# Optimization experiments

Measured on AMD Instinct MI355X. Metric: run time of the kernel, lower is better.

## Reference

```python
import jax, jax.numpy as jnp
import numpy as np

N_NODES = 100000
N_EDGES = 1600000
IN_CH = 128
HID = 128
OUT_CH = 10
NUM_LAYERS = 3
NUM_GRAPHS = 512


def _glorot(key, shape):
    fan_in, fan_out = shape[0], shape[1]
    lim = jnp.sqrt(6.0 / (fan_in + fan_out))
    return jax.random.uniform(key, shape, jnp.float32, -lim, lim)


def setup_inputs() -> dict:
    key = jax.random.key(0)
    ks = jax.random.split(key, 20)
    inp = {}
    inp["x"] = jax.random.normal(ks[0], (N_NODES, IN_CH), jnp.float32)
    inp["edge_index"] = jax.random.randint(ks[1], (2, N_EDGES), 0, N_NODES, jnp.int64)
    inp["batch"] = jnp.sort(jax.random.randint(ks[2], (N_NODES,), 0, NUM_GRAPHS, jnp.int64))
    # GIN layer MLP params: Linear(in, hid) -> ReLU -> Linear(hid, hid)
    kidx = 3
    for l in range(NUM_LAYERS):
        d_in = IN_CH if l == 0 else HID
        inp[f"w1_{l}"] = _glorot(ks[kidx], (d_in, HID)); kidx += 1
        inp[f"b1_{l}"] = jnp.zeros((HID,), jnp.float32)
        inp[f"w2_{l}"] = _glorot(ks[kidx], (HID, HID)); kidx += 1
        inp[f"b2_{l}"] = jnp.zeros((HID,), jnp.float32)
    inp["lin_w"] = _glorot(ks[kidx], (HID, OUT_CH))
    inp["lin_b"] = jnp.zeros((OUT_CH,), jnp.float32)
    return inp


def _gin_forward(x, src, dst, batch, layer_params, lin_w, lin_b):
    h = x
    n_layers = len(layer_params)
    for i, (w1, b1, w2, b2) in enumerate(layer_params):
        # GINConv: (1 + eps) * h + sum_{j in N(i)} h_j, eps = 0
        agg = jax.ops.segment_sum(h[src], dst, num_segments=N_NODES)
        z = h + agg
        # MLP: Linear -> ReLU -> Linear
        h = jnp.maximum(z @ w1 + b1, 0.0) @ w2 + b2
        if i < n_layers - 1:  # inter-layer ReLU (PyG BasicGNN act)
            h = jnp.maximum(h, 0.0)
    # global_add_pool over batch ids -> [NUM_GRAPHS, HID]
    pooled = jax.ops.segment_sum(h, batch, num_segments=NUM_GRAPHS)
    # dropout(p=0.5) is identity in eval mode
    return pooled @ lin_w + lin_b


def reference(x, edge_index, batch,
              w1_0, b1_0, w2_0, b2_0,
              w1_1, b1_1, w2_1, b2_1,
              w1_2, b1_2, w2_2, b2_2,
              lin_w, lin_b):
    src, dst = edge_index[0], edge_index[1]
    layer_params = [(w1_0, b1_0, w2_0, b2_0),
                    (w1_1, b1_1, w2_1, b2_1),
                    (w1_2, b1_2, w2_2, b2_2)]
    return _gin_forward(x, src, dst, batch, layer_params, lin_w, lin_b)
```

## Files before the change

kernel.cpp:

```cpp
#include <hip/hip_runtime.h>

#define CH 128
#define OUTC 10
#define NB2 512
#define BSHIFT 8
#define BCAP2 5120
#define PCHUNK 2048
#define PQ2 132
#define FBM 64

typedef __attribute__((ext_vector_type(8))) short short8;
typedef __attribute__((ext_vector_type(4))) short short4v;
typedef __attribute__((ext_vector_type(16))) float f32x16;
typedef __attribute__((ext_vector_type(2))) float f32x2;


__device__ inline unsigned short f2bf(float f) {
    unsigned u = __builtin_bit_cast(unsigned, f);
    u += 0x7fffu + ((u >> 16) & 1u);
    return (unsigned short)(u >> 16);
}
__device__ inline float bflo(unsigned u) { return __builtin_bit_cast(float, u << 16); }
__device__ inline float bfhi(unsigned u) { return __builtin_bit_cast(float, u & 0xffff0000u); }

__device__ inline f32x2 bf2(unsigned u) {
    return (f32x2){__builtin_bit_cast(float, u << 16),
                   __builtin_bit_cast(float, u & 0xffff0000u)};
}

__device__ inline void acc8(f32x2* a, const uint4& v) {
    a[0] += bf2(v.x);
    a[1] += bf2(v.y);
    a[2] += bf2(v.z);
    a[3] += bf2(v.w);
}


struct WPtrs { const float* s[6]; unsigned short* d[6]; };

__global__ void prep_part_kernel(const int* __restrict__ src, const int* __restrict__ dst,
                                 int* __restrict__ bucketCnt, unsigned* __restrict__ pairs, int E,
                                 int nPartBlk,
                                 const float4* __restrict__ x4, uint2* __restrict__ xb, int n4,
                                 int nConvBlk, WPtrs p,
                                 uint4* __restrict__ pooled4, int nPooled4) {
    __shared__ int hist[NB2];
    __shared__ int base[NB2];
    __shared__ int cur[NB2];
    int tid = threadIdx.x;
    int b = blockIdx.x;

    if (b < nPartBlk) {
        int e0 = b * PCHUNK;
        hist[tid] = 0; hist[tid + 256] = 0;
        __syncthreads();
        #pragma unroll
        for (int i = 0; i < PCHUNK / 256; ++i) {
            int e = e0 + tid + i * 256;
            if (e < E) atomicAdd(&hist[dst[e] >> BSHIFT], 1);
        }
        __syncthreads();
        #pragma unroll
        for (int k = 0; k < 2; ++k) {
            int t2 = tid + k * 256;
            int c = hist[t2];
            base[t2] = (c > 0) ? atomicAdd(&bucketCnt[t2], c) : 0;
            cur[t2] = 0;
        }
        __syncthreads();
        #pragma unroll
        for (int i = 0; i < PCHUNK / 256; ++i) {
            int e = e0 + tid + i * 256;
            if (e < E) {
                int d = dst[e];
                int bkt = d >> BSHIFT;
                int pos = base[bkt] + atomicAdd(&cur[bkt], 1);
                if (pos < BCAP2)
                    pairs[bkt * BCAP2 + pos] = ((unsigned)(d & 255) << 17) | (unsigned)src[e];
            }
        }
    } else if (b < nPartBlk + nConvBlk) {
        int i = (b - nPartBlk) * 256 + tid;
        if (i < n4) {
            float4 v = x4[i];
            uint2 o;
            o.x = (unsigned)f2bf(v.x) | ((unsigned)f2bf(v.y) << 16);
            o.y = (unsigned)f2bf(v.z) | ((unsigned)f2bf(v.w) << 16);
            xb[i] = o;
        }
    } else if (b < nPartBlk + nConvBlk + 384) {
        int bb = b - nPartBlk - nConvBlk;
        int m = bb >> 6;
        int i = (bb & 63) * 256 + tid;
        int j = i & 7;
        int l = (i >> 3) & 63;
        int k0 = (i >> 9) & 7;
        int ct = (i >> 12) & 3;
        int k = k0 * 16 + ((l >> 5) << 3) + j;
        int nn = ct * 32 + (l & 31);
        p.d[m][i] = f2bf(p.s[m][k * CH + nn]);
    } else {
        int i = (b - nPartBlk - nConvBlk - 384) * 256 + tid;
        if (i < nPooled4) pooled4[i] = make_uint4(0, 0, 0, 0);
    }
}


__launch_bounds__(512)
__global__ void build_csr_kernel(const unsigned* __restrict__ pairs, const int* __restrict__ bucketCnt,
                                 int* __restrict__ offs, int* __restrict__ csr, int N) {
    __shared__ int bsm[NB2];
    __shared__ int ldeg[256];
    __shared__ int s0[256], s1[256];
    __shared__ int lexc[256];
    __shared__ int lcur[256];
    __shared__ int lcsr[BCAP2];

    int b = blockIdx.x;
    int node0 = b << BSHIFT;
    if (node0 >= N) return;
    int nLocal = min(256, N - node0);
    int tid = threadIdx.x;

    bsm[tid] = bucketCnt[tid];
    __syncthreads();
    for (int off = 1; off < NB2; off <<= 1) {
        int t = (tid >= off) ? bsm[tid - off] : 0;
        __syncthreads();
        bsm[tid] += t;
        __syncthreads();
    }
    int cnt = min(bucketCnt[b], BCAP2);
    int gbase = bsm[b] - bucketCnt[b];

    if (tid < 256) ldeg[tid] = 0;
    __syncthreads();
    for (int i = tid; i < cnt; i += 512)
        atomicAdd(&ldeg[pairs[b * BCAP2 + i] >> 17], 1);
    __syncthreads();

    if (tid < 256) s0[tid] = ldeg[tid];
    __syncthreads();
    int* sp = s0; int* dp = s1;
    for (int off = 1; off < 256; off <<= 1) {
        if (tid < 256) dp[tid] = sp[tid] + ((tid >= off) ? sp[tid - off] : 0);
        __syncthreads();
        int* t = sp; sp = dp; dp = t;
    }
    if (tid < 256) {
        int ex = sp[tid] - ldeg[tid];
        lexc[tid] = ex;
        lcur[tid] = ex;
    }
    __syncthreads();

    for (int i = tid; i < cnt; i += 512) {
        unsigned w = pairs[b * BCAP2 + i];
        int ppos = atomicAdd(&lcur[w >> 17], 1);
        lcsr[ppos] = (int)(w & 0x1ffffu);
    }
    __syncthreads();

    for (int i = tid; i < cnt; i += 512) csr[gbase + i] = lcsr[i];
    for (int i = tid; i < nLocal; i += 512) offs[node0 + i] = gbase + lexc[i];
    if (tid == 0 && node0 + nLocal == N) offs[N] = gbase + cnt;
}


template <int L, int RELU, int POOL>
__launch_bounds__(512)
__global__ void fused_gin_kernel(const uint4* __restrict__ h4,
                                 const int* __restrict__ offs, const int* __restrict__ csr,
                                 const unsigned short* __restrict__ w1s, const float* __restrict__ b1,
                                 const unsigned short* __restrict__ w2s, const float* __restrict__ b2,
                                 unsigned short* __restrict__ hout,
                                 const int* __restrict__ batch, float* __restrict__ pooled,
                                 int n) {
    __shared__ __align__(16) unsigned short zs[FBM * PQ2];

    int tid = threadIdx.x;
    int row0 = blockIdx.x * FBM;

    {
        int gl = tid & 15;
        int grp = tid >> 4;
        #pragma unroll
        for (int it = 0; it < 2; ++it) {
            int rr = grp + 32 * it;
            int node = row0 + rr;
            unsigned o0 = 0, o1 = 0, o2 = 0, o3 = 0;
            if (node < n) {
                int beg = offs[node], end = offs[node + 1];
                f32x2 a[4];
                uint4 self = h4[node * 16 + gl];
                a[0] = bf2(self.x);
                a[1] = bf2(self.y);
                a[2] = bf2(self.z);
                a[3] = bf2(self.w);
                int e = beg;
                int elim = beg + ((end - beg) & ~3);
                if (e < elim) {
                    int s0 = csr[e], s1 = csr[e + 1], s2 = csr[e + 2], s3 = csr[e + 3];
                    for (; e + 8 <= elim; e += 4) {
                        uint4 v0 = h4[s0 * 16 + gl];
                        uint4 v1 = h4[s1 * 16 + gl];
                        uint4 v2 = h4[s2 * 16 + gl];
                        uint4 v3 = h4[s3 * 16 + gl];
                        int t0 = csr[e + 4], t1 = csr[e + 5], t2 = csr[e + 6], t3 = csr[e + 7];
                        acc8(a, v0); acc8(a, v1); acc8(a, v2); acc8(a, v3);
                        s0 = t0; s1 = t1; s2 = t2; s3 = t3;
                    }
                    {
                        uint4 v0 = h4[s0 * 16 + gl];
                        uint4 v1 = h4[s1 * 16 + gl];
                        uint4 v2 = h4[s2 * 16 + gl];
                        uint4 v3 = h4[s3 * 16 + gl];
                        acc8(a, v0); acc8(a, v1); acc8(a, v2); acc8(a, v3);
                        e += 4;
                    }
                }
                for (; e < end; ++e) {
                    uint4 v = h4[csr[e] * 16 + gl];
                    acc8(a, v);
                }
                o0 = (unsigned)f2bf(a[0][0]) | ((unsigned)f2bf(a[0][1]) << 16);
                o1 = (unsigned)f2bf(a[1][0]) | ((unsigned)f2bf(a[1][1]) << 16);
                o2 = (unsigned)f2bf(a[2][0]) | ((unsigned)f2bf(a[2][1]) << 16);
                o3 = (unsigned)f2bf(a[3][0]) | ((unsigned)f2bf(a[3][1]) << 16);
            }
            *(uint2*)&zs[rr * PQ2 + gl * 8]     = make_uint2(o0, o1);
            *(uint2*)&zs[rr * PQ2 + gl * 8 + 4] = make_uint2(o2, o3);
        }
    }
    __syncthreads();

    int wv = tid >> 6;
    int lane = tid & 63;
    int l31 = lane & 31;
    int kh = lane >> 5;
    int rt = wv & 1;
    int ct = wv >> 1;
    int arow = rt * 32 + l31;

    f32x16 acc;
    {
        float bv = b1[ct * 32 + l31];
        #pragma unroll
        for (int r = 0; r < 16; ++r) acc[r] = bv;
    }
    #pragma unroll
    for (int k0 = 0; k0 < 8; ++k0) {
        short8 afr;
        {
            short4v lo = *(const short4v*)&zs[arow * PQ2 + k0 * 16 + kh * 8];
            short4v hi = *(const short4v*)&zs[arow * PQ2 + k0 * 16 + kh * 8 + 4];
            afr = (short8){lo[0], lo[1], lo[2], lo[3], hi[0], hi[1], hi[2], hi[3]};
        }
        short8 bfr = *(const short8*)&w1s[(((ct * 8 + k0) * 64) + lane) * 8];
        acc = __builtin_amdgcn_mfma_f32_32x32x16_bf16(afr, bfr, acc, 0, 0, 0);
    }
    __syncthreads();

    #pragma unroll
    for (int reg = 0; reg < 16; ++reg) {
        int crow = (reg & 3) + 8 * (reg >> 2) + 4 * kh;
        zs[(rt * 32 + crow) * PQ2 + ct * 32 + l31] = f2bf(fmaxf(acc[reg], 0.f));
    }
    __syncthreads();

    {
        float bv = b2[ct * 32 + l31];
        #pragma unroll
        for (int r = 0; r < 16; ++r) acc[r] = bv;
    }
    #pragma unroll
    for (int k0 = 0; k0 < 8; ++k0) {
        short8 afr;
        {
            short4v lo = *(const short4v*)&zs[arow * PQ2 + k0 * 16 + kh * 8];
            short4v hi = *(const short4v*)&zs[arow * PQ2 + k0 * 16 + kh * 8 + 4];
            afr = (short8){lo[0], lo[1], lo[2], lo[3], hi[0], hi[1], hi[2], hi[3]};
        }
        short8 bfr = *(const short8*)&w2s[(((ct * 8 + k0) * 64) + lane) * 8];
        acc = __builtin_amdgcn_mfma_f32_32x32x16_bf16(afr, bfr, acc, 0, 0, 0);
    }
    __syncthreads();

    #pragma unroll
    for (int reg = 0; reg < 16; ++reg) {
        int crow = (reg & 3) + 8 * (reg >> 2) + 4 * kh;
        float v = acc[reg];
        if (RELU) v = fmaxf(v, 0.f);
        zs[(rt * 32 + crow) * PQ2 + ct * 32 + l31] = f2bf(v);
    }
    __syncthreads();

    if (!POOL) {
        for (int i = tid; i < FBM * 16; i += 512) {
            int r = i >> 4, c = i & 15;
            int row = row0 + r;
            if (row < n) {
                uint2 a2 = *(const uint2*)&zs[r * PQ2 + c * 8];
                uint2 b2v = *(const uint2*)&zs[r * PQ2 + c * 8 + 4];
                ((uint4*)hout)[row * 16 + c] = make_uint4(a2.x, a2.y, b2v.x, b2v.y);
            }
        }
    } else {
        int c2 = tid & 63;
        int rs = tid >> 6;
        float a0 = 0.f, a1 = 0.f;
        int prevg = -1;
        #pragma unroll
        for (int i = 0; i < FBM / 8; ++i) {
            int r = rs + 8 * i;
            int row = row0 + r;
            if (row >= n) break;
            int g = batch[row];
            if (g != prevg) {
                if (prevg >= 0) {
                    atomicAdd(&pooled[prevg * CH + 2 * c2], a0);
                    atomicAdd(&pooled[prevg * CH + 2 * c2 + 1], a1);
                }
                prevg = g; a0 = 0.f; a1 = 0.f;
            }
            unsigned v = *(const unsigned*)&zs[r * PQ2 + c2 * 2];
            a0 += bflo(v); a1 += bfhi(v);
        }
        if (prevg >= 0) {
            atomicAdd(&pooled[prevg * CH + 2 * c2], a0);
            atomicAdd(&pooled[prevg * CH + 2 * c2 + 1], a1);
        }
    }
}


__global__ void final_linear_kernel(const float* __restrict__ pooled, const float* __restrict__ lin_w,
                                    const float* __restrict__ lin_b, float* __restrict__ out) {
    int g = blockIdx.x;
    int tid = threadIdx.x;
    __shared__ float pl[CH];
    pl[tid] = pooled[g * CH + tid];
    __syncthreads();
    if (tid < OUTC) {
        float a = lin_b[tid];
        #pragma unroll 16
        for (int c = 0; c < CH; ++c) a = fmaf(pl[c], lin_w[c * OUTC + tid], a);
        out[g * OUTC + tid] = a;
    }
}


static inline size_t aln(size_t x) { return (x + 255) & ~size_t(255); }

extern "C" void kernel_launch(void* const* d_in, const int* in_sizes, int n_in,
                              void* d_out, int out_size, void* d_ws, size_t ws_size,
                              hipStream_t stream) {
    const float* x      = (const float*)d_in[0];
    const int*   ei     = (const int*)d_in[1];
    const int*   batch  = (const int*)d_in[2];
    const float* w1[3]  = {(const float*)d_in[3], (const float*)d_in[7],  (const float*)d_in[11]};
    const float* b1[3]  = {(const float*)d_in[4], (const float*)d_in[8],  (const float*)d_in[12]};
    const float* w2[3]  = {(const float*)d_in[5], (const float*)d_in[9],  (const float*)d_in[13]};
    const float* b2[3]  = {(const float*)d_in[6], (const float*)d_in[10], (const float*)d_in[14]};
    const float* lin_w  = (const float*)d_in[15];
    const float* lin_b  = (const float*)d_in[16];
    float* out = (float*)d_out;

    int E = in_sizes[1] / 2;
    int N = in_sizes[2];
    int n_graphs = out_size / OUTC;
    const int* src = ei;
    const int* dst = ei + E;

    char* p = (char*)d_ws;
    int* bucketCnt  = (int*)p; p += aln(NB2 * 4);
    unsigned* pairs = (unsigned*)p; p += aln((size_t)NB2 * BCAP2 * 4);
    int* offs       = (int*)p; p += aln((size_t)(N + 1) * 4);
    int* csr        = (int*)p; p += aln((size_t)E * 4);
    unsigned short* xb = (unsigned short*)p; p += aln((size_t)N * CH * 2);
    unsigned short* hA = (unsigned short*)p; p += aln((size_t)N * CH * 2);
    unsigned short* hB = (unsigned short*)p; p += aln((size_t)N * CH * 2);
    float* pooled = (float*)p; p += aln((size_t)n_graphs * CH * 4);
    unsigned short* wt[6];
    for (int i = 0; i < 6; ++i) { wt[i] = (unsigned short*)p; p += aln((size_t)CH * CH * 2); }
    (void)ws_size; (void)n_in;

    hipMemsetAsync(bucketCnt, 0, NB2 * 4, stream);

    int n4 = N * CH / 4;
    int nConvBlk = (n4 + 255) / 256;
    int nPartBlk = (E + PCHUNK - 1) / PCHUNK;
    int nPooled4 = n_graphs * CH / 4;
    int nZeroBlk = (nPooled4 + 255) / 256;
    WPtrs wp;
    for (int l = 0; l < 3; ++l) {
        wp.s[2 * l] = w1[l];     wp.d[2 * l] = wt[2 * l];
        wp.s[2 * l + 1] = w2[l]; wp.d[2 * l + 1] = wt[2 * l + 1];
    }
    prep_part_kernel<<<nPartBlk + nConvBlk + 384 + nZeroBlk, 256, 0, stream>>>(
        src, dst, bucketCnt, pairs, E, nPartBlk,
        (const float4*)x, (uint2*)xb, n4, nConvBlk, wp,
        (uint4*)pooled, nPooled4);

    build_csr_kernel<<<NB2, 512, 0, stream>>>(pairs, bucketCnt, offs, csr, N);

    int fblk = (N + FBM - 1) / FBM;

    fused_gin_kernel<0, 1, 0><<<fblk, 512, 0, stream>>>((const uint4*)xb, offs, csr,
        wt[0], b1[0], wt[1], b2[0], hA, batch, pooled, N);
    fused_gin_kernel<1, 1, 0><<<fblk, 512, 0, stream>>>((const uint4*)hA, offs, csr,
        wt[2], b1[1], wt[3], b2[1], hB, batch, pooled, N);
    fused_gin_kernel<2, 0, 1><<<fblk, 512, 0, stream>>>((const uint4*)hB, offs, csr,
        wt[4], b1[2], wt[5], b2[2], (unsigned short*)nullptr, batch, pooled, N);

    final_linear_kernel<<<n_graphs, CH, 0, stream>>>(pooled, lin_w, lin_b, out);
}
```

Measured before the change: 377.1 us.

## Merge all GIN stages into one persistent cooperative kernel with grid syncs

Replaces the six separate launches (partition/prep, CSR build, three fused GIN layers, final linear) with a single cooperative persistent kernel. Grid-wide syncs separate the stages, and blocks loop over work items in grid-stride fashion. The aim is to remove per-launch overhead and the tail gaps between kernels. The cost is lower occupancy: shared memory is sized for the largest stage, and the grid is capped by the occupancy query. It also adds grid-sync overhead, and the aggregation loop drops its software-pipelined csr prefetch.

Measured after the change: 872.9 us. +131.5%, slower.

```diff
diff --git a/kernel.cpp b/kernel.cpp
--- a/kernel.cpp
+++ b/kernel.cpp
@@ -1,4 +1,7 @@
 #include <hip/hip_runtime.h>
+#include <hip/hip_cooperative_groups.h>
+
+namespace cg = cooperative_groups;
 
 #define CH 128
 #define OUTC 10
@@ -8,6 +11,7 @@
 #define PCHUNK 2048
 #define PQ2 132
 #define FBM 64
+#define TPB 512
 
 typedef __attribute__((ext_vector_type(8))) short short8;
 typedef __attribute__((ext_vector_type(4))) short short4v;
@@ -36,203 +40,158 @@
 }
 
 
-struct WPtrs { const float* s[6]; unsigned short* d[6]; };
-
-__global__ void prep_part_kernel(const int* __restrict__ src, const int* __restrict__ dst,
-                                 int* __restrict__ bucketCnt, unsigned* __restrict__ pairs, int E,
-                                 int nPartBlk,
-                                 const float4* __restrict__ x4, uint2* __restrict__ xb, int n4,
-                                 int nConvBlk, WPtrs p,
-                                 uint4* __restrict__ pooled4, int nPooled4) {
-    __shared__ int hist[NB2];
-    __shared__ int base[NB2];
-    __shared__ int cur[NB2];
+struct MegaP {
+    const int* src; const int* dst; int E;
+    int* bucketCnt; unsigned* pairs;
+    int* offs; int* csr; int N;
+    const float4* x4; unsigned short* xb; int n4;
+    const float* wsrc[6]; unsigned short* wdst[6];
+    const float* b1v[3]; const float* b2v[3];
+    unsigned short* hA; unsigned short* hB;
+    const int* batch; float* pooled; int nPooled4;
+    int nGraphs; const float* lin_w; const float* lin_b; float* out;
+};
+
+
+__launch_bounds__(TPB, 8)
+__global__ void mega_kernel(MegaP P) {
+    cg::grid_group gg = cg::this_grid();
+    __shared__ __align__(16) int smem[6912];
+
     int tid = threadIdx.x;
     int b = blockIdx.x;
-
-    if (b < nPartBlk) {
-        int e0 = b * PCHUNK;
-        hist[tid] = 0; hist[tid + 256] = 0;
+    int grid = (int)gridDim.x;
+
+    int nPartBlk = (P.E + PCHUNK - 1) / PCHUNK;
+    for (int pb = b; pb < nPartBlk; pb += grid) {
+        int* hist = smem;
+        int* base = smem + NB2;
+        int* cur  = smem + 2 * NB2;
+        int e0 = pb * PCHUNK;
+        hist[tid] = 0;
         __syncthreads();
         #pragma unroll
-        for (int i = 0; i < PCHUNK / 256; ++i) {
-            int e = e0 + tid + i * 256;
-            if (e < E) atomicAdd(&hist[dst[e] >> BSHIFT], 1);
+        for (int i = 0; i < PCHUNK / TPB; ++i) {
+            int e = e0 + tid + i * TPB;
+            if (e < P.E) atomicAdd(&hist[P.dst[e] >> BSHIFT], 1);
+        }
+        __syncthreads();
+        {
+            int c = hist[tid];
+            base[tid] = (c > 0) ? atomicAdd(&P.bucketCnt[tid], c) : 0;
+            cur[tid] = 0;
         }
         __syncthreads();
         #pragma unroll
-        for (int k = 0; k < 2; ++k) {
-            int t2 = tid + k * 256;
-            int c = hist[t2];
-            base[t2] = (c > 0) ? atomicAdd(&bucketCnt[t2], c) : 0;
-            cur[t2] = 0;
-        }
-        __syncthreads();
-        #pragma unroll
-        for (int i = 0; i < PCHUNK / 256; ++i) {
-            int e = e0 + tid + i * 256;
-            if (e < E) {
-                int d = dst[e];
+        for (int i = 0; i < PCHUNK / TPB; ++i) {
+            int e = e0 + tid + i * TPB;
+            if (e < P.E) {
+                int d = P.dst[e];
                 int bkt = d >> BSHIFT;
                 int pos = base[bkt] + atomicAdd(&cur[bkt], 1);
                 if (pos < BCAP2)
-                    pairs[bkt * BCAP2 + pos] = ((unsigned)(d & 255) << 17) | (unsigned)src[e];
-            }
-        }
-    } else if (b < nPartBlk + nConvBlk) {
-        int i = (b - nPartBlk) * 256 + tid;
-        if (i < n4) {
-            float4 v = x4[i];
+                    P.pairs[bkt * BCAP2 + pos] = ((unsigned)(d & 255) << 17) | (unsigned)P.src[e];
+            }
+        }
+        __syncthreads();
+    }
+    {
+        int wtot = 6 * 16384 + P.nPooled4;
+        int rb = grid - 1 - b;
+        for (int i = rb * TPB + tid; i < wtot; i += grid * TPB) {
+            if (i < 6 * 16384) {
+                int m = i >> 14;
+                int im = i & 16383;
+                int j = im & 7;
+                int l = (im >> 3) & 63;
+                int k0 = (im >> 9) & 7;
+                int ct = (im >> 12) & 3;
+                int k = k0 * 16 + ((l >> 5) << 3) + j;
+                int nn = ct * 32 + (l & 31);
+                P.wdst[m][im] = f2bf(P.wsrc[m][k * CH + nn]);
+            } else {
+                ((uint4*)P.pooled)[i - 6 * 16384] = make_uint4(0, 0, 0, 0);
+            }
+        }
+    }
+    gg.sync();
+
+    int nCsr = (P.N + 255) >> BSHIFT;
+    for (int cb = b; cb < nCsr; cb += grid) {
+        int* bsm  = smem;
+        int* ldeg = smem + NB2;
+        int* s0   = smem + NB2 + 256;
+        int* s1   = s0 + 256;
+        int* lexc = s1 + 256;
+        int* lcur = lexc + 256;
+        int* lcsr = lcur + 256;
+        int node0 = cb << BSHIFT;
+        int nLocal = min(256, P.N - node0);
+
+        bsm[tid] = P.bucketCnt[tid];
+        __syncthreads();
+        for (int off = 1; off < NB2; off <<= 1) {
+            int t = (tid >= off) ? bsm[tid - off] : 0;
+            __syncthreads();
+            bsm[tid] += t;
+            __syncthreads();
+        }
+        int cnt = min(P.bucketCnt[cb], BCAP2);
+        int gbase = bsm[cb] - P.bucketCnt[cb];
+
+        if (tid < 256) ldeg[tid] = 0;
+        __syncthreads();
+        for (int i = tid; i < cnt; i += TPB)
+            atomicAdd(&ldeg[P.pairs[cb * BCAP2 + i] >> 17], 1);
+        __syncthreads();
+
+        if (tid < 256) s0[tid] = ldeg[tid];
+        __syncthreads();
+        int* sp = s0; int* dp = s1;
+        for (int off = 1; off < 256; off <<= 1) {
+            if (tid < 256) dp[tid] = sp[tid] + ((tid >= off) ? sp[tid - off] : 0);
+            __syncthreads();
+            int* t = sp; sp = dp; dp = t;
+        }
+        if (tid < 256) {
+            int ex = sp[tid] - ldeg[tid];
+            lexc[tid] = ex;
+            lcur[tid] = ex;
+        }
+        __syncthreads();
+
+        for (int i = tid; i < cnt; i += TPB) {
+            unsigned w = P.pairs[cb * BCAP2 + i];
+            int ppos = atomicAdd(&lcur[w >> 17], 1);
+            lcsr[ppos] = (int)(w & 0x1ffffu);
+        }
+        __syncthreads();
+
+        for (int i = tid; i < cnt; i += TPB) P.csr[gbase + i] = lcsr[i];
+        for (int i = tid; i < nLocal; i += TPB) P.offs[node0 + i] = gbase + lexc[i];
+        if (tid == 0 && node0 + nLocal == P.N) P.offs[P.N] = gbase + cnt;
+        __syncthreads();
+    }
+    {
+        int i0, stride;
+        if (grid > nCsr) {
+            if (b >= nCsr) { i0 = (b - nCsr) * TPB + tid; stride = (grid - nCsr) * TPB; }
+            else           { i0 = P.n4; stride = 1; }
+        } else {
+            i0 = b * TPB + tid; stride = grid * TPB;
+        }
+        for (int i = i0; i < P.n4; i += stride) {
+            float4 v = P.x4[i];
             uint2 o;
             o.x = (unsigned)f2bf(v.x) | ((unsigned)f2bf(v.y) << 16);
             o.y = (unsigned)f2bf(v.z) | ((unsigned)f2bf(v.w) << 16);
-            xb[i] = o;
-        }
-    } else if (b < nPartBlk + nConvBlk + 384) {
-        int bb = b - nPartBlk - nConvBlk;
-        int m = bb >> 6;
-        int i = (bb & 63) * 256 + tid;
-        int j = i & 7;
-        int l = (i >> 3) & 63;
-        int k0 = (i >> 9) & 7;
-        int ct = (i >> 12) & 3;
-        int k = k0 * 16 + ((l >> 5) << 3) + j;
-        int nn = ct * 32 + (l & 31);
-        p.d[m][i] = f2bf(p.s[m][k * CH + nn]);
-    } else {
-        int i = (b - nPartBlk - nConvBlk - 384) * 256 + tid;
-        if (i < nPooled4) pooled4[i] = make_uint4(0, 0, 0, 0);
-    }
-}
-
-
-__launch_bounds__(512)
-__global__ void build_csr_kernel(const unsigned* __restrict__ pairs, const int* __restrict__ bucketCnt,
-                                 int* __restrict__ offs, int* __restrict__ csr, int N) {
-    __shared__ int bsm[NB2];
-    __shared__ int ldeg[256];
-    __shared__ int s0[256], s1[256];
-    __shared__ int lexc[256];
-    __shared__ int lcur[256];
-    __shared__ int lcsr[BCAP2];
-
-    int b = blockIdx.x;
-    int node0 = b << BSHIFT;
-    if (node0 >= N) return;
-    int nLocal = min(256, N - node0);
-    int tid = threadIdx.x;
-
-    bsm[tid] = bucketCnt[tid];
-    __syncthreads();
-    for (int off = 1; off < NB2; off <<= 1) {
-        int t = (tid >= off) ? bsm[tid - off] : 0;
-        __syncthreads();
-        bsm[tid] += t;
-        __syncthreads();
-    }
-    int cnt = min(bucketCnt[b], BCAP2);
-    int gbase = bsm[b] - bucketCnt[b];
-
-    if (tid < 256) ldeg[tid] = 0;
-    __syncthreads();
-    for (int i = tid; i < cnt; i += 512)
-        atomicAdd(&ldeg[pairs[b * BCAP2 + i] >> 17], 1);
-    __syncthreads();
-
-    if (tid < 256) s0[tid] = ldeg[tid];
-    __syncthreads();
-    int* sp = s0; int* dp = s1;
-    for (int off = 1; off < 256; off <<= 1) {
-        if (tid < 256) dp[tid] = sp[tid] + ((tid >= off) ? sp[tid - off] : 0);
-        __syncthreads();
-        int* t = sp; sp = dp; dp = t;
-    }
-    if (tid < 256) {
-        int ex = sp[tid] - ldeg[tid];
-        lexc[tid] = ex;
-        lcur[tid] = ex;
-    }
-    __syncthreads();
-
-    for (int i = tid; i < cnt; i += 512) {
-        unsigned w = pairs[b * BCAP2 + i];
-        int ppos = atomicAdd(&lcur[w >> 17], 1);
-        lcsr[ppos] = (int)(w & 0x1ffffu);
-    }
-    __syncthreads();
-
-    for (int i = tid; i < cnt; i += 512) csr[gbase + i] = lcsr[i];
-    for (int i = tid; i < nLocal; i += 512) offs[node0 + i] = gbase + lexc[i];
-    if (tid == 0 && node0 + nLocal == N) offs[N] = gbase + cnt;
-}
-
-
-template <int L, int RELU, int POOL>
-__launch_bounds__(512)
-__global__ void fused_gin_kernel(const uint4* __restrict__ h4,
-                                 const int* __restrict__ offs, const int* __restrict__ csr,
-                                 const unsigned short* __restrict__ w1s, const float* __restrict__ b1,
-                                 const unsigned short* __restrict__ w2s, const float* __restrict__ b2,
-                                 unsigned short* __restrict__ hout,
-                                 const int* __restrict__ batch, float* __restrict__ pooled,
-                                 int n) {
-    __shared__ __align__(16) unsigned short zs[FBM * PQ2];
-
-    int tid = threadIdx.x;
-    int row0 = blockIdx.x * FBM;
-
-    {
-        int gl = tid & 15;
-        int grp = tid >> 4;
-        #pragma unroll
-        for (int it = 0; it < 2; ++it) {
-            int rr = grp + 32 * it;
-            int node = row0 + rr;
-            unsigned o0 = 0, o1 = 0, o2 = 0, o3 = 0;
-            if (node < n) {
-                int beg = offs[node], end = offs[node + 1];
-                f32x2 a[4];
-                uint4 self = h4[node * 16 + gl];
-                a[0] = bf2(self.x);
-                a[1] = bf2(self.y);
-                a[2] = bf2(self.z);
-                a[3] = bf2(self.w);
-                int e = beg;
-                int elim = beg + ((end - beg) & ~3);
-                if (e < elim) {
-                    int s0 = csr[e], s1 = csr[e + 1], s2 = csr[e + 2], s3 = csr[e + 3];
-                    for (; e + 8 <= elim; e += 4) {
-                        uint4 v0 = h4[s0 * 16 + gl];
-                        uint4 v1 = h4[s1 * 16 + gl];
-                        uint4 v2 = h4[s2 * 16 + gl];
-                        uint4 v3 = h4[s3 * 16 + gl];
-                        int t0 = csr[e + 4], t1 = csr[e + 5], t2 = csr[e + 6], t3 = csr[e + 7];
-                        acc8(a, v0); acc8(a, v1); acc8(a, v2); acc8(a, v3);
-                        s0 = t0; s1 = t1; s2 = t2; s3 = t3;
-                    }
-                    {
-                        uint4 v0 = h4[s0 * 16 + gl];
-                        uint4 v1 = h4[s1 * 16 + gl];
-                        uint4 v2 = h4[s2 * 16 + gl];
-                        uint4 v3 = h4[s3 * 16 + gl];
-                        acc8(a, v0); acc8(a, v1); acc8(a, v2); acc8(a, v3);
-                        e += 4;
-                    }
-                }
-                for (; e < end; ++e) {
-                    uint4 v = h4[csr[e] * 16 + gl];
-                    acc8(a, v);
-                }
-                o0 = (unsigned)f2bf(a[0][0]) | ((unsigned)f2bf(a[0][1]) << 16);
-                o1 = (unsigned)f2bf(a[1][0]) | ((unsigned)f2bf(a[1][1]) << 16);
-                o2 = (unsigned)f2bf(a[2][0]) | ((unsigned)f2bf(a[2][1]) << 16);
-                o3 = (unsigned)f2bf(a[3][0]) | ((unsigned)f2bf(a[3][1]) << 16);
-            }
-            *(uint2*)&zs[rr * PQ2 + gl * 8]     = make_uint2(o0, o1);
-            *(uint2*)&zs[rr * PQ2 + gl * 8 + 4] = make_uint2(o2, o3);
-        }
-    }
-    __syncthreads();
+            ((uint2*)P.xb)[i] = o;
+        }
+    }
+    gg.sync();
+
+    unsigned short* zs = (unsigned short*)smem;
+    int NT = (P.N + FBM - 1) / FBM;
 
     int wv = tid >> 6;
     int lane = tid & 63;
@@ -242,110 +201,165 @@
     int ct = wv >> 1;
     int arow = rt * 32 + l31;
 
-    f32x16 acc;
-    {
-        float bv = b1[ct * 32 + l31];
-        #pragma unroll
-        for (int r = 0; r < 16; ++r) acc[r] = bv;
-    }
-    #pragma unroll
-    for (int k0 = 0; k0 < 8; ++k0) {
-        short8 afr;
-        {
-            short4v lo = *(const short4v*)&zs[arow * PQ2 + k0 * 16 + kh * 8];
-            short4v hi = *(const short4v*)&zs[arow * PQ2 + k0 * 16 + kh * 8 + 4];
-            afr = (short8){lo[0], lo[1], lo[2], lo[3], hi[0], hi[1], hi[2], hi[3]};
-        }
-        short8 bfr = *(const short8*)&w1s[(((ct * 8 + k0) * 64) + lane) * 8];
-        acc = __builtin_amdgcn_mfma_f32_32x32x16_bf16(afr, bfr, acc, 0, 0, 0);
-    }
-    __syncthreads();
-
-    #pragma unroll
-    for (int reg = 0; reg < 16; ++reg) {
-        int crow = (reg & 3) + 8 * (reg >> 2) + 4 * kh;
-        zs[(rt * 32 + crow) * PQ2 + ct * 32 + l31] = f2bf(fmaxf(acc[reg], 0.f));
-    }
-    __syncthreads();
-
-    {
-        float bv = b2[ct * 32 + l31];
-        #pragma unroll
-        for (int r = 0; r < 16; ++r) acc[r] = bv;
-    }
-    #pragma unroll
-    for (int k0 = 0; k0 < 8; ++k0) {
-        short8 afr;
-        {
-            short4v lo = *(const short4v*)&zs[arow * PQ2 + k0 * 16 + kh * 8];
-            short4v hi = *(const short4v*)&zs[arow * PQ2 + k0 * 16 + kh * 8 + 4];
-            afr = (short8){lo[0], lo[1], lo[2], lo[3], hi[0], hi[1], hi[2], hi[3]};
-        }
-        short8 bfr = *(const short8*)&w2s[(((ct * 8 + k0) * 64) + lane) * 8];
-        acc = __builtin_amdgcn_mfma_f32_32x32x16_bf16(afr, bfr, acc, 0, 0, 0);
-    }
-    __syncthreads();
-
-    #pragma unroll
-    for (int reg = 0; reg < 16; ++reg) {
-        int crow = (reg & 3) + 8 * (reg >> 2) + 4 * kh;
-        float v = acc[reg];
-        if (RELU) v = fmaxf(v, 0.f);
-        zs[(rt * 32 + crow) * PQ2 + ct * 32 + l31] = f2bf(v);
-    }
-    __syncthreads();
-
-    if (!POOL) {
-        for (int i = tid; i < FBM * 16; i += 512) {
-            int r = i >> 4, c = i & 15;
-            int row = row0 + r;
-            if (row < n) {
-                uint2 a2 = *(const uint2*)&zs[r * PQ2 + c * 8];
-                uint2 b2v = *(const uint2*)&zs[r * PQ2 + c * 8 + 4];
-                ((uint4*)hout)[row * 16 + c] = make_uint4(a2.x, a2.y, b2v.x, b2v.y);
-            }
-        }
-    } else {
-        int c2 = tid & 63;
-        int rs = tid >> 6;
-        float a0 = 0.f, a1 = 0.f;
-        int prevg = -1;
-        #pragma unroll
-        for (int i = 0; i < FBM / 8; ++i) {
-            int r = rs + 8 * i;
-            int row = row0 + r;
-            if (row >= n) break;
-            int g = batch[row];
-            if (g != prevg) {
+    for (int l = 0; l < 3; ++l) {
+        const uint4* h4 = (l == 0) ? (const uint4*)P.xb
+                        : (l == 1) ? (const uint4*)P.hA : (const uint4*)P.hB;
+        unsigned short* hout = (l == 0) ? P.hA : P.hB;
+        const unsigned short* w1s = P.wdst[2 * l];
+        const unsigned short* w2s = P.wdst[2 * l + 1];
+        const float* b1 = P.b1v[l];
+        const float* b2 = P.b2v[l];
+        int relu = (l < 2) ? 1 : 0;
+        int pool = (l == 2) ? 1 : 0;
+
+        for (int t = b; t < NT; t += grid) {
+            int row0 = t * FBM;
+
+            {
+                int gl = tid & 15;
+                int grp = tid >> 4;
+                #pragma unroll
+                for (int it2 = 0; it2 < 2; ++it2) {
+                    int rr = grp + 32 * it2;
+                    int node = row0 + rr;
+                    unsigned o0 = 0, o1 = 0, o2 = 0, o3 = 0;
+                    if (node < P.N) {
+                        int beg = P.offs[node], end = P.offs[node + 1];
+                        f32x2 a[4];
+                        uint4 self = h4[node * 16 + gl];
+                        a[0] = bf2(self.x);
+                        a[1] = bf2(self.y);
+                        a[2] = bf2(self.z);
+                        a[3] = bf2(self.w);
+                        int e = beg;
+                        for (; e + 4 <= end; e += 4) {
+                            int s0i = P.csr[e], s1i = P.csr[e + 1], s2i = P.csr[e + 2], s3i = P.csr[e + 3];
+                            uint4 v0 = h4[s0i * 16 + gl];
+                            uint4 v1 = h4[s1i * 16 + gl];
+                            uint4 v2 = h4[s2i * 16 + gl];
+                            uint4 v3 = h4[s3i * 16 + gl];
+                            acc8(a, v0); acc8(a, v1); acc8(a, v2); acc8(a, v3);
+                        }
+                        for (; e < end; ++e) {
+                            uint4 v = h4[P.csr[e] * 16 + gl];
+                            acc8(a, v);
+                        }
+                        o0 = (unsigned)f2bf(a[0][0]) | ((unsigned)f2bf(a[0][1]) << 16);
+                        o1 = (unsigned)f2bf(a[1][0]) | ((unsigned)f2bf(a[1][1]) << 16);
+                        o2 = (unsigned)f2bf(a[2][0]) | ((unsigned)f2bf(a[2][1]) << 16);
+                        o3 = (unsigned)f2bf(a[3][0]) | ((unsigned)f2bf(a[3][1]) << 16);
+                    }
+                    *(uint2*)&zs[rr * PQ2 + gl * 8]     = make_uint2(o0, o1);
+                    *(uint2*)&zs[rr * PQ2 + gl * 8 + 4] = make_uint2(o2, o3);
+                }
+            }
+            __syncthreads();
+
+            f32x16 acc;
+            {
+                float bv = b1[ct * 32 + l31];
+                #pragma unroll
+                for (int r = 0; r < 16; ++r) acc[r] = bv;
+            }
+            #pragma unroll
+            for (int k0 = 0; k0 < 8; ++k0) {
+                short8 afr;
+                {
+                    short4v lo = *(const short4v*)&zs[arow * PQ2 + k0 * 16 + kh * 8];
+                    short4v hi = *(const short4v*)&zs[arow * PQ2 + k0 * 16 + kh * 8 + 4];
+                    afr = (short8){lo[0], lo[1], lo[2], lo[3], hi[0], hi[1], hi[2], hi[3]};
+                }
+                short8 bfr = *(const short8*)&w1s[(((ct * 8 + k0) * 64) + lane) * 8];
+                acc = __builtin_amdgcn_mfma_f32_32x32x16_bf16(afr, bfr, acc, 0, 0, 0);
+            }
+            __syncthreads();
+
+            #pragma unroll
+            for (int reg = 0; reg < 16; ++reg) {
+                int crow = (reg & 3) + 8 * (reg >> 2) + 4 * kh;
+                zs[(rt * 32 + crow) * PQ2 + ct * 32 + l31] = f2bf(fmaxf(acc[reg], 0.f));
+            }
+            __syncthreads();
+
+            {
+                float bv = b2[ct * 32 + l31];
+                #pragma unroll
+                for (int r = 0; r < 16; ++r) acc[r] = bv;
+            }
+            #pragma unroll
+            for (int k0 = 0; k0 < 8; ++k0) {
+                short8 afr;
+                {
+                    short4v lo = *(const short4v*)&zs[arow * PQ2 + k0 * 16 + kh * 8];
+                    short4v hi = *(const short4v*)&zs[arow * PQ2 + k0 * 16 + kh * 8 + 4];
+                    afr = (short8){lo[0], lo[1], lo[2], lo[3], hi[0], hi[1], hi[2], hi[3]};
+                }
+                short8 bfr = *(const short8*)&w2s[(((ct * 8 + k0) * 64) + lane) * 8];
+                acc = __builtin_amdgcn_mfma_f32_32x32x16_bf16(afr, bfr, acc, 0, 0, 0);
+            }
+            __syncthreads();
+
+            #pragma unroll
+            for (int reg = 0; reg < 16; ++reg) {
+                int crow = (reg & 3) + 8 * (reg >> 2) + 4 * kh;
+                float v = acc[reg];
+                if (relu) v = fmaxf(v, 0.f);
+                zs[(rt * 32 + crow) * PQ2 + ct * 32 + l31] = f2bf(v);
+            }
+            __syncthreads();
+
+            if (!pool) {
+                for (int i = tid; i < FBM * 16; i += TPB) {
+                    int r = i >> 4, c = i & 15;
+                    int row = row0 + r;
+                    if (row < P.N) {
+                        uint2 a2 = *(const uint2*)&zs[r * PQ2 + c * 8];
+                        uint2 b2u = *(const uint2*)&zs[r * PQ2 + c * 8 + 4];
+                        ((uint4*)hout)[row * 16 + c] = make_uint4(a2.x, a2.y, b2u.x, b2u.y);
+                    }
+                }
+            } else {
+                int c2 = tid & 63;
+                int rs = tid >> 6;
+                float a0 = 0.f, a1 = 0.f;
+                int prevg = -1;
+                #pragma unroll
+                for (int i = 0; i < FBM / 8; ++i) {
+                    int r = rs + 8 * i;
+                    int row = row0 + r;
+                    if (row >= P.N) break;
+                    int g = P.batch[row];
+                    if (g != prevg) {
+                        if (prevg >= 0) {
+                            atomicAdd(&P.pooled[prevg * CH + 2 * c2], a0);
+                            atomicAdd(&P.pooled[prevg * CH + 2 * c2 + 1], a1);
+                        }
+                        prevg = g; a0 = 0.f; a1 = 0.f;
+                    }
+                    unsigned v = *(const unsigned*)&zs[r * PQ2 + c2 * 2];
+                    a0 += bflo(v); a1 += bfhi(v);
+                }
                 if (prevg >= 0) {
-                    atomicAdd(&pooled[prevg * CH + 2 * c2], a0);
-                    atomicAdd(&pooled[prevg * CH + 2 * c2 + 1], a1);
-                }
-                prevg = g; a0 = 0.f; a1 = 0.f;
-            }
-            unsigned v = *(const unsigned*)&zs[r * PQ2 + c2 * 2];
-            a0 += bflo(v); a1 += bfhi(v);
-        }
-        if (prevg >= 0) {
-            atomicAdd(&pooled[prevg * CH + 2 * c2], a0);
-            atomicAdd(&pooled[prevg * CH + 2 * c2 + 1], a1);
-        }
-    }
-}
-
-
-__global__ void final_linear_kernel(const float* __restrict__ pooled, const float* __restrict__ lin_w,
-                                    const float* __restrict__ lin_b, float* __restrict__ out) {
-    int g = blockIdx.x;
-    int tid = threadIdx.x;
-    __shared__ float pl[CH];
-    pl[tid] = pooled[g * CH + tid];
-    __syncthreads();
-    if (tid < OUTC) {
-        float a = lin_b[tid];
-        #pragma unroll 16
-        for (int c = 0; c < CH; ++c) a = fmaf(pl[c], lin_w[c * OUTC + tid], a);
-        out[g * OUTC + tid] = a;
+                    atomicAdd(&P.pooled[prevg * CH + 2 * c2], a0);
+                    atomicAdd(&P.pooled[prevg * CH + 2 * c2 + 1], a1);
+                }
+            }
+            __syncthreads();
+        }
+        gg.sync();
+    }
+
+    for (int gb = b; gb < P.nGraphs; gb += grid) {
+        float* pl = (float*)smem;
+        if (tid < CH) pl[tid] = P.pooled[gb * CH + tid];
+        __syncthreads();
+        if (tid < OUTC) {
+            float a = P.lin_b[tid];
+            #pragma unroll 16
+            for (int c = 0; c < CH; ++c) a = fmaf(pl[c], P.lin_w[c * OUTC + tid], a);
+            P.out[gb * OUTC + tid] = a;
+        }
+        __syncthreads();
     }
 }
 
@@ -387,31 +401,28 @@
 
     hipMemsetAsync(bucketCnt, 0, NB2 * 4, stream);
 
-    int n4 = N * CH / 4;
-    int nConvBlk = (n4 + 255) / 256;
-    int nPartBlk = (E + PCHUNK - 1) / PCHUNK;
-    int nPooled4 = n_graphs * CH / 4;
-    int nZeroBlk = (nPooled4 + 255) / 256;
-    WPtrs wp;
+    MegaP P;
+    P.src = src; P.dst = dst; P.E = E;
+    P.bucketCnt = bucketCnt; P.pairs = pairs;
+    P.offs = offs; P.csr = csr; P.N = N;
+    P.x4 = (const float4*)x; P.xb = xb; P.n4 = N * CH / 4;
     for (int l = 0; l < 3; ++l) {
-        wp.s[2 * l] = w1[l];     wp.d[2 * l] = wt[2 * l];
-        wp.s[2 * l + 1] = w2[l]; wp.d[2 * l + 1] = wt[2 * l + 1];
-    }
-    prep_part_kernel<<<nPartBlk + nConvBlk + 384 + nZeroBlk, 256, 0, stream>>>(
-        src, dst, bucketCnt, pairs, E, nPartBlk,
-        (const float4*)x, (uint2*)xb, n4, nConvBlk, wp,
-        (uint4*)pooled, nPooled4);
-
-    build_csr_kernel<<<NB2, 512, 0, stream>>>(pairs, bucketCnt, offs, csr, N);
-
-    int fblk = (N + FBM - 1) / FBM;
-
-    fused_gin_kernel<0, 1, 0><<<fblk, 512, 0, stream>>>((const uint4*)xb, offs, csr,
-        wt[0], b1[0], wt[1], b2[0], hA, batch, pooled, N);
-    fused_gin_kernel<1, 1, 0><<<fblk, 512, 0, stream>>>((const uint4*)hA, offs, csr,
-        wt[2], b1[1], wt[3], b2[1], hB, batch, pooled, N);
-    fused_gin_kernel<2, 0, 1><<<fblk, 512, 0, stream>>>((const uint4*)hB, offs, csr,
-        wt[4], b1[2], wt[5], b2[2], (unsigned short*)nullptr, batch, pooled, N);
-
-    final_linear_kernel<<<n_graphs, CH, 0, stream>>>(pooled, lin_w, lin_b, out);
+        P.wsrc[2 * l] = w1[l];     P.wdst[2 * l] = wt[2 * l];
+        P.wsrc[2 * l + 1] = w2[l]; P.wdst[2 * l + 1] = wt[2 * l + 1];
+        P.b1v[l] = b1[l]; P.b2v[l] = b2[l];
+    }
+    P.hA = hA; P.hB = hB;
+    P.batch = batch; P.pooled = pooled; P.nPooled4 = n_graphs * CH / 4;
+    P.nGraphs = n_graphs; P.lin_w = lin_w; P.lin_b = lin_b; P.out = out;
+
+    int maxB = 0;
+    hipOccupancyMaxActiveBlocksPerMultiprocessor(&maxB, mega_kernel, TPB, 0);
+    if (maxB < 1) maxB = 1;
+    long long grid = (long long)maxB * 256;
+    if (grid > 2048) grid = 2048;
+    if (grid < 256) grid = 256;
+
+    void* kargs[] = { (void*)&P };
+    hipLaunchCooperativeKernel(reinterpret_cast<void*>(mega_kernel),
+                               dim3((unsigned)grid), dim3(TPB), kargs, 0, stream);
 }
```
